# Performance work log

Measured on AMD Instinct MI355X. Metric: run time of the kernel, lower is better.

Reference implementation:

```python
import jax, jax.numpy as jnp
import numpy as np

N_ELEC = 8192   # electrons (nodes)
N_NUC = 512     # nuclei
EMB = 256       # embedding_dim
KER = 256       # kernel_dim
DF = 64         # dist_feat_dim
MID = 128       # round(sqrt(DF*KER)), log-interpolated hidden width of w-MLP
E = 131072      # edges per edge type


def _ssp(x):
    # shifted softplus, deepqmc default activation: log(0.5*exp(x) + 0.5)
    return jax.nn.softplus(x) - jnp.log(2.0)


def setup_inputs() -> dict:
    key = jax.random.key(0)
    ks = jax.random.split(key, 24)
    def nrm(k, shape, scale):
        return jax.random.normal(k, shape, dtype=jnp.float32) * scale
    inp = {}
    inp['electrons'] = nrm(ks[0], (N_ELEC, EMB), 1.0)
    inp['nuclei'] = nrm(ks[1], (N_NUC, KER), 1.0)
    for i, lbl in enumerate(['same', 'anti', 'n']):
        inp[f'dist_{lbl}'] = jax.random.uniform(ks[2 + i], (E, DF), dtype=jnp.float32)
        inp[f'w1_{lbl}'] = nrm(ks[5 + i], (DF, MID), DF ** -0.5)
        inp[f'b1_{lbl}'] = jnp.zeros((MID,), jnp.float32)
        inp[f'w2_{lbl}'] = nrm(ks[8 + i], (MID, KER), MID ** -0.5)
        inp[f'g_{lbl}'] = nrm(ks[11 + i], (KER, EMB), KER ** -0.5)
    inp['h_w'] = nrm(ks[14], (EMB, KER), EMB ** -0.5)
    inp['senders_same'] = jax.random.randint(ks[15], (E,), 0, N_ELEC)
    inp['senders_anti'] = jax.random.randint(ks[16], (E,), 0, N_ELEC)
    inp['senders_n'] = jax.random.randint(ks[17], (E,), 0, N_NUC)
    inp['receivers_same'] = jax.random.randint(ks[18], (E,), 0, N_ELEC)
    inp['receivers_anti'] = jax.random.randint(ks[19], (E,), 0, N_ELEC)
    inp['receivers_n'] = jax.random.randint(ks[20], (E,), 0, N_ELEC)
    return inp


def reference(electrons, nuclei, dist_same, dist_anti, dist_n,
              w1_same, b1_same, w2_same, w1_anti, b1_anti, w2_anti,
              w1_n, b1_n, w2_n, g_same, g_anti, g_n, h_w,
              senders_same, senders_anti, senders_n,
              receivers_same, receivers_anti, receivers_n):
    def w_mlp(d, w1, b1, w2):
        # MLP with ('log', 2) hidden layers: linear+bias -> SSP -> last linear (no bias)
        return _ssp(d @ w1 + b1) @ w2

    # per-edge filters from distance features: [E, KER]
    we_same = w_mlp(dist_same, w1_same, b1_same, w2_same)
    we_anti = w_mlp(dist_anti, w1_anti, b1_anti, w2_anti)
    we_n = w_mlp(dist_n, w1_n, b1_n, w2_n)

    # shared h (single bias-free linear) on gathered sender electrons: [E, KER]
    hx_same = electrons[senders_same] @ h_w
    hx_anti = electrons[senders_anti] @ h_w

    weh_same = we_same * hx_same
    weh_anti = we_anti * hx_anti
    weh_n = we_n * nuclei[senders_n]

    # scatter-sum messages to receiver electrons: [N_ELEC, KER]
    z_same = jax.ops.segment_sum(weh_same, receivers_same, num_segments=N_ELEC)
    z_anti = jax.ops.segment_sum(weh_anti, receivers_anti, num_segments=N_ELEC)
    z_n = jax.ops.segment_sum(weh_n, receivers_n, num_segments=N_ELEC)

    # per-label g (single bias-free linear) + residual update, order matches original
    return electrons + (z_n @ g_n + z_same @ g_same + z_anti @ g_anti)
```

## Files before the change

kernel.cpp:

```cpp
#include <hip/hip_runtime.h>
#include <stdint.h>


#define N_ELEC 8192
#define N_NUC  512
#define EMB    256
#define KER    256
#define DF     64
#define MID    128
#define NEDGE  131072
#define RPS    8256
#define CSTR   272

using u16 = unsigned short;
using u64 = unsigned long long;
typedef short short8 __attribute__((ext_vector_type(8)));
typedef float f32x4 __attribute__((ext_vector_type(4)));

__device__ __forceinline__ float bf2f(u16 h) {
  return __uint_as_float(((unsigned)h) << 16);
}
__device__ __forceinline__ u16 f2bf(float f) {
  unsigned u = __float_as_uint(f);
  return (u16)((u + 0x7FFFu + ((u >> 16) & 1u)) >> 16);
}
__device__ __forceinline__ unsigned pkbf(float a, float b) {
  return ((unsigned)f2bf(b) << 16) | (unsigned)f2bf(a);
}
__device__ __forceinline__ float ssp_fast(float x) {
  const float e = __expf(-fabsf(x));
  return fmaxf(x, 0.f) + __logf(fmaf(0.5f, e, 0.5f));
}

__device__ __forceinline__ void bar_lds() {
  __builtin_amdgcn_sched_barrier(0);
  asm volatile("s_waitcnt lgkmcnt(0)" ::: "memory");
  __builtin_amdgcn_s_barrier();
  __builtin_amdgcn_sched_barrier(0);
}

__device__ __forceinline__ void stage_t64(const char* g0, long stride,
                                          char* lds, int tid) {
  const int l = tid & 63, w = tid >> 6;
  const int r = w * 16 + (l >> 2);
  const int cb = (l & 3) * 16;
  __builtin_amdgcn_global_load_lds(
      (const __attribute__((address_space(1))) unsigned*)(g0 +
                                                          (long)r * stride +
                                                          cb),
      (__attribute__((address_space(3))) unsigned*)(lds + w * 1024), 16, 0, 0);
}
__device__ __forceinline__ void stage_f64(const float* g0, int stride_e,
                                          int kt, char* lds, int tid) {
#pragma unroll
  for (int k = 0; k < 4; ++k) {
    const int idx2 = k * 256 + tid;
    const int row = idx2 >> 4, cp = idx2 & 15;
    const float2 v = *(const float2*)(g0 + (long)row * stride_e + kt + cp * 2);
    *(unsigned*)(lds + row * 64 + cp * 4) = pkbf(v.x, v.y);
  }
}
template <bool A_F32>
__device__ __forceinline__ void gemm64(const char* A0, long as_bytes,
                                       const float* Af, int as_elems,
                                       const char* B0, long bs, int K,
                                       char* As, char* Bs, f32x4 acc[2][2],
                                       int tid) {
  const int l = tid & 63, lane15 = l & 15, quad = l >> 4, wv = tid >> 6;
  const int mw = (wv >> 1) * 32, nw = (wv & 1) * 32;
  for (int kt = 0; kt < K; kt += 32) {
    if (A_F32)
      stage_f64(Af, as_elems, kt, As, tid);
    else
      stage_t64(A0 + (long)kt * 2, as_bytes, As, tid);
    stage_t64(B0 + (long)kt * 2, bs, Bs, tid);
    __syncthreads();
    short8 af[2], bf[2];
#pragma unroll
    for (int i = 0; i < 2; ++i) {
      af[i] = *(const short8*)(As + (mw + i * 16 + lane15) * 64 + quad * 16);
      bf[i] = *(const short8*)(Bs + (nw + i * 16 + lane15) * 64 + quad * 16);
    }
#pragma unroll
    for (int mi = 0; mi < 2; ++mi)
#pragma unroll
      for (int ni = 0; ni < 2; ++ni)
        acc[mi][ni] = __builtin_amdgcn_mfma_f32_16x16x32_bf16(
            af[mi], bf[ni], acc[mi][ni], 0, 0, 0);
    __syncthreads();
  }
}

__global__ __launch_bounds__(256) void k_setup(
    const float* h_w, const float* w1s, const float* w1a, const float* w1n,
    const float* w2s, const float* w2a, const float* w2n, const float* gs,
    const float* ga, const float* gn, u16* hwT, u16* w1T, u16* w2T, u16* gT,
    float4* z, int* cnt) {
  const int b = blockIdx.x;
  if (b < 6144) {
    z[b * 256 + threadIdx.x] = (float4){0.f, 0.f, 0.f, 0.f};
    return;
  }
  if (b < 6240) {
    cnt[(b - 6144) * 256 + threadIdx.x] = 0;
    return;
  }
  int i = (b - 6240) * 256 + threadIdx.x;
  if (i < 65536) {
    int n = i >> 8, k = i & 255;
    hwT[i] = f2bf(h_w[k * 256 + n]);
    return;
  }
  int j = i - 65536;
  if (j < 24576) {
    int t = j >> 13, jj = j & 8191, n = jj >> 6, k = jj & 63;
    const float* w1 = t == 0 ? w1s : (t == 1 ? w1a : w1n);
    w1T[j] = f2bf(w1[k * 128 + n]);
    return;
  }
  j -= 24576;
  if (j < 98304) {
    int t = j >> 15, jj = j & 32767, n = jj >> 7, k = jj & 127;
    const float* w2 = t == 0 ? w2s : (t == 1 ? w2a : w2n);
    w2T[j] = f2bf(w2[k * 256 + n]);
    return;
  }
  j -= 98304;
  if (j < 196608) {
    int n = j / 768, q = j % 768, t = q >> 8, k = q & 255;
    const float* g = t == 0 ? gs : (t == 1 ? ga : gn);
    gT[j] = f2bf(g[k * 256 + n]);
  }
}

__global__ __launch_bounds__(256) void k_hist(const int* r0, const int* r1,
                                              const int* r2, int* cnt) {
  const int t = blockIdx.z;
  const int* rcv = t == 0 ? r0 : (t == 1 ? r1 : r2);
  const int e = blockIdx.x * 256 + threadIdx.x;
  atomicAdd(&cnt[t * N_ELEC + rcv[e]], 1);
}

__global__ __launch_bounds__(256) void k_scan(const int* cnt, int* rowptr,
                                              int* cursor) {
  const int t = blockIdx.x, tid = threadIdx.x;
  __shared__ int part[256];
  const int* c = cnt + t * N_ELEC;
  int s = 0;
#pragma unroll
  for (int i = 0; i < 32; ++i) s += c[tid * 32 + i];
  part[tid] = s;
  __syncthreads();
  for (int off = 1; off < 256; off <<= 1) {
    int v = (tid >= off) ? part[tid - off] : 0;
    __syncthreads();
    part[tid] += v;
    __syncthreads();
  }
  int run = (tid == 0) ? 0 : part[tid - 1];
  int* rp = rowptr + t * RPS;
  int* cu = cursor + t * N_ELEC;
  for (int i = 0; i < 32; ++i) {
    rp[tid * 32 + i] = run;
    cu[tid * 32 + i] = run;
    run += c[tid * 32 + i];
  }
  if (tid == 255) rp[N_ELEC] = run;
}

__global__ __launch_bounds__(256) void k_place(const int* r0, const int* r1,
                                               const int* r2, const int* s0,
                                               const int* s1, const int* s2,
                                               int* cursor, u64* pk) {
  const int t = blockIdx.z;
  const int* rcv = t == 0 ? r0 : (t == 1 ? r1 : r2);
  const int* snd = t == 0 ? s0 : (t == 1 ? s1 : s2);
  const int e = blockIdx.x * 256 + threadIdx.x;
  const int rr = rcv[e];
  const int pos = atomicAdd(&cursor[t * N_ELEC + rr], 1);
  pk[t * NEDGE + pos] =
      (u64)(unsigned)e | ((u64)(unsigned)snd[e] << 17) | ((u64)(unsigned)rr << 30);
}

__global__ __launch_bounds__(256) void k_he(const float* elec, const u16* hwT,
                                            u16* he) {
  __shared__ char As[4096], Bs[4096];
  f32x4 acc[2][2];
#pragma unroll
  for (int i = 0; i < 2; ++i)
#pragma unroll
    for (int j = 0; j < 2; ++j) acc[i][j] = (f32x4){0.f, 0.f, 0.f, 0.f};
  const int m0 = blockIdx.x * 64, n0 = blockIdx.y * 64;
  gemm64<true>(nullptr, 0, elec + (long)m0 * 256, 256,
               (const char*)hwT + (long)n0 * 512, 512, 256, As, Bs, acc,
               threadIdx.x);
  const int l = threadIdx.x & 63, lane15 = l & 15, quad = l >> 4,
            wv = threadIdx.x >> 6;
  const int mw = (wv >> 1) * 32, nw = (wv & 1) * 32;
#pragma unroll
  for (int mi = 0; mi < 2; ++mi)
#pragma unroll
    for (int r = 0; r < 4; ++r) {
      const int row = m0 + mw + mi * 16 + quad * 4 + r;
#pragma unroll
      for (int ni = 0; ni < 2; ++ni) {
        const int col = n0 + nw + ni * 16 + lane15;
        he[row * 256 + col] = f2bf(acc[mi][ni][r]);
      }
    }
}

__global__ __launch_bounds__(256, 5) void k_edge(
    const float* d0, const float* d1, const float* d2, const float* b0,
    const float* b1p, const float* b2, const u16* w1T, const u16* w2T,
    const u16* he, const float* nucf, const u64* pk, float* z) {
  __shared__ char mid[64 * CSTR];
  __shared__ char hc[32 * CSTR];
  __shared__ int snd_l[64], rcv_l[64];

  const int t = blockIdx.z;
  const int m0 = blockIdx.x * 64;
  const int tid = threadIdx.x;
  const float* dist = t == 0 ? d0 : (t == 1 ? d1 : d2);
  const float* bias = t == 0 ? b0 : (t == 1 ? b1p : b2);
  const u16* w1t = w1T + t * 8192;
  const u16* w2t = w2T + t * 32768;
  const bool is_nuc = (t == 2);
  const u64* pkt = pk + (size_t)t * NEDGE + m0;

  if (tid < 64) {
    const u64 rec = pkt[tid];
    snd_l[tid] = (int)((rec >> 17) & 0x1FFFu);
    rcv_l[tid] = (int)(rec >> 30);
  }

  int rows[2];
#pragma unroll
  for (int s = 0; s < 2; ++s)
    rows[s] = (int)(pkt[(s * 256 + tid) >> 3] & 0x1FFFFu);
#pragma unroll
  for (int j = 0; j < 2; ++j)
#pragma unroll
    for (int s = 0; s < 2; ++s) {
      const int idx = s * 256 + tid, row = idx >> 3, ch = idx & 7;
      const float4 v =
          *(const float4*)(dist + (long)rows[s] * 64 + j * 32 + ch * 4);
      uint2 p;
      p.x = pkbf(v.x, v.y);
      p.y = pkbf(v.z, v.w);
      *(uint2*)(mid + j * 4096 + row * 64 + ch * 8) = p;
    }
  bar_lds();

  const int l = tid & 63, lane15 = l & 15, quad = l >> 4, wv = tid >> 6;
  const int mw = (wv >> 1) * 32;
  const int nw = (wv & 1) * 64;

  f32x4 acc[2][4];
#pragma unroll
  for (int i = 0; i < 2; ++i)
#pragma unroll
    for (int j = 0; j < 4; ++j) acc[i][j] = (f32x4){0.f, 0.f, 0.f, 0.f};
#pragma unroll
  for (int j = 0; j < 2; ++j) {
    short8 af[2], bf[4];
#pragma unroll
    for (int i = 0; i < 2; ++i)
      af[i] = *(const short8*)(mid + j * 4096 + (mw + i * 16 + lane15) * 64 +
                               quad * 16);
#pragma unroll
    for (int i = 0; i < 4; ++i)
      bf[i] = *(const short8*)(w1t + (nw + i * 16 + lane15) * 64 + j * 32 +
                               quad * 8);
#pragma unroll
    for (int mi = 0; mi < 2; ++mi)
#pragma unroll
      for (int ni = 0; ni < 4; ++ni)
        acc[mi][ni] = __builtin_amdgcn_mfma_f32_16x16x32_bf16(
            af[mi], bf[ni], acc[mi][ni], 0, 0, 0);
  }
  bar_lds();

#pragma unroll
  for (int mi = 0; mi < 2; ++mi)
#pragma unroll
    for (int r = 0; r < 4; ++r) {
      const int row = mw + mi * 16 + quad * 4 + r;
#pragma unroll
      for (int ni = 0; ni < 4; ++ni) {
        const int col = nw + ni * 16 + lane15;
        const float x = acc[mi][ni][r] + bias[col];
        *(u16*)(mid + row * CSTR + col * 2) = f2bf(ssp_fast(x));
      }
    }
  bar_lds();

  for (int n0 = 0; n0 < 256; n0 += 128) {
#pragma unroll
    for (int i = 0; i < 2; ++i)
#pragma unroll
      for (int j = 0; j < 4; ++j) acc[i][j] = (f32x4){0.f, 0.f, 0.f, 0.f};
#pragma unroll
    for (int kt = 0; kt < 128; kt += 32) {
      short8 af[2], bf[4];
#pragma unroll
      for (int i = 0; i < 2; ++i)
        af[i] = *(const short8*)(mid + (mw + i * 16 + lane15) * CSTR + kt * 2 +
                                 quad * 16);
#pragma unroll
      for (int i = 0; i < 4; ++i)
        bf[i] = *(const short8*)(w2t + (n0 + nw + i * 16 + lane15) * 128 + kt +
                                 quad * 8);
#pragma unroll
      for (int mi = 0; mi < 2; ++mi)
#pragma unroll
        for (int ni = 0; ni < 4; ++ni)
          acc[mi][ni] = __builtin_amdgcn_mfma_f32_16x16x32_bf16(
              af[mi], bf[ni], acc[mi][ni], 0, 0, 0);
    }

#pragma unroll
    for (int h = 0; h < 2; ++h) {
      const int rbase = h * 32;
      if (!is_nuc) {
#pragma unroll
        for (int c = 0; c < 2; ++c) {
          const int chunk = c * 256 + tid;
          const int row = chunk >> 4, off = chunk & 15;
          const uint4 v =
              *(const uint4*)((const char*)he +
                              (size_t)snd_l[rbase + row] * 512 + n0 * 2 +
                              off * 16);
          *(uint4*)(hc + row * CSTR + off * 16) = v;
        }
      } else {
#pragma unroll
        for (int c = 0; c < 2; ++c) {
          const int chunk = c * 256 + tid;
          const int row = chunk >> 4, off = chunk & 15;
          const char* src = (const char*)nucf +
                            (size_t)snd_l[rbase + row] * 1024 + n0 * 4 +
                            off * 32;
          const float4 a = *(const float4*)src;
          const float4 b = *(const float4*)(src + 16);
          uint4 p;
          p.x = pkbf(a.x, a.y);
          p.y = pkbf(a.z, a.w);
          p.z = pkbf(b.x, b.y);
          p.w = pkbf(b.z, b.w);
          *(uint4*)(hc + row * CSTR + off * 16) = p;
        }
      }
      bar_lds();

      if ((wv >> 1) == h) {
#pragma unroll
        for (int mi = 0; mi < 2; ++mi)
#pragma unroll
          for (int r = 0; r < 4; ++r) {
            const int lrow = mi * 16 + quad * 4 + r;
#pragma unroll
            for (int ni = 0; ni < 4; ++ni) {
              const int col = nw + ni * 16 + lane15;
              u16* p = (u16*)(hc + lrow * CSTR) + col;
              *p = f2bf(acc[mi][ni][r] * bf2f(*p));
            }
          }
      }
      bar_lds();

      if (wv < 2) {
        const int cp = l;
        const int rbeg = wv * 16, rend = rbeg + 16;
        float a0 = 0.f, a1 = 0.f;
        int cur = rcv_l[rbase + rbeg];
#pragma unroll
        for (int i = 0; i < 16; ++i) {
          const int row = rbeg + i;
          const unsigned p = *(const unsigned*)(hc + row * CSTR + cp * 4);
          a0 += __uint_as_float(p << 16);
          a1 += __uint_as_float(p & 0xffff0000u);
          const int nxt = (i + 1 < 16) ? rcv_l[rbase + row + 1] : -1;
          if (nxt != cur) {
            float* zp = z + (size_t)cur * 768 + t * 256 + n0 + cp * 2;
            unsafeAtomicAdd(zp, a0);
            unsafeAtomicAdd(zp + 1, a1);
            a0 = a1 = 0.f;
            cur = nxt;
          }
        }
      }
      bar_lds();
    }
  }
}

__global__ __launch_bounds__(256) void k_final(const float* z, const u16* gT,
                                               const float* elec, float* out) {
  __shared__ char As[4096], Bs[4096];
  f32x4 acc[2][2];
#pragma unroll
  for (int i = 0; i < 2; ++i)
#pragma unroll
    for (int j = 0; j < 2; ++j) acc[i][j] = (f32x4){0.f, 0.f, 0.f, 0.f};
  const int m0 = blockIdx.x * 64, n0 = blockIdx.y * 64;
  gemm64<true>(nullptr, 0, z + (long)m0 * 768, 768,
               (const char*)gT + (long)n0 * 1536, 1536, 768, As, Bs, acc,
               threadIdx.x);
  const int l = threadIdx.x & 63, lane15 = l & 15, quad = l >> 4,
            wv = threadIdx.x >> 6;
  const int mw = (wv >> 1) * 32, nw = (wv & 1) * 32;
#pragma unroll
  for (int mi = 0; mi < 2; ++mi)
#pragma unroll
    for (int r = 0; r < 4; ++r) {
      const int row = m0 + mw + mi * 16 + quad * 4 + r;
#pragma unroll
      for (int ni = 0; ni < 2; ++ni) {
        const int col = n0 + nw + ni * 16 + lane15;
        out[row * 256 + col] = acc[mi][ni][r] + elec[row * 256 + col];
      }
    }
}

extern "C" void kernel_launch(void* const* d_in, const int* in_sizes, int n_in,
                              void* d_out, int out_size, void* d_ws,
                              size_t ws_size, hipStream_t stream) {
  int I_dist[3], I_w1[3], I_b1[3], I_w2[3], I_g[3], I_hw;
  if (in_sizes[3] == 64 * 128) {
    for (int t = 0; t < 3; ++t) {
      I_dist[t] = 2 + t * 5 + 0;
      I_w1[t] = 2 + t * 5 + 1;
      I_b1[t] = 2 + t * 5 + 2;
      I_w2[t] = 2 + t * 5 + 3;
      I_g[t] = 2 + t * 5 + 4;
    }
    I_hw = 17;
  } else {
    I_dist[0] = 2; I_dist[1] = 3; I_dist[2] = 4;
    I_w1[0] = 5;  I_b1[0] = 6;  I_w2[0] = 7;
    I_w1[1] = 8;  I_b1[1] = 9;  I_w2[1] = 10;
    I_w1[2] = 11; I_b1[2] = 12; I_w2[2] = 13;
    I_g[0] = 14; I_g[1] = 15; I_g[2] = 16;
    I_hw = 17;
  }
  const int I_snd[3] = {18, 19, 20};
  const int I_rcv[3] = {21, 22, 23};

  char* ws = (char*)d_ws;
  u16* he = (u16*)(ws + 0);
  u16* hwT = (u16*)(ws + 4194304);
  u16* w1T = (u16*)(ws + 4325376);
  u16* w2T = (u16*)(ws + 4374528);
  u16* gT = (u16*)(ws + 4571136);
  float* z = (float*)(ws + 4964352);
  int* cnt = (int*)(ws + 30130176);
  int* rowptr = (int*)(ws + 30228480);
  int* cursor = (int*)(ws + 30327552);
  u64* pk = (u64*)(ws + 30425856);

  const float* elec = (const float*)d_in[0];
  const float* nuc = (const float*)d_in[1];
  const int* s0 = (const int*)d_in[I_snd[0]];
  const int* s1 = (const int*)d_in[I_snd[1]];
  const int* s2 = (const int*)d_in[I_snd[2]];
  const int* r0 = (const int*)d_in[I_rcv[0]];
  const int* r1 = (const int*)d_in[I_rcv[1]];
  const int* r2 = (const int*)d_in[I_rcv[2]];

  k_setup<<<7744, 256, 0, stream>>>(
      (const float*)d_in[I_hw], (const float*)d_in[I_w1[0]],
      (const float*)d_in[I_w1[1]], (const float*)d_in[I_w1[2]],
      (const float*)d_in[I_w2[0]], (const float*)d_in[I_w2[1]],
      (const float*)d_in[I_w2[2]], (const float*)d_in[I_g[0]],
      (const float*)d_in[I_g[1]], (const float*)d_in[I_g[2]], hwT, w1T, w2T,
      gT, (float4*)z, cnt);

  k_hist<<<dim3(NEDGE / 256, 1, 3), 256, 0, stream>>>(r0, r1, r2, cnt);
  k_scan<<<3, 256, 0, stream>>>(cnt, rowptr, cursor);
  k_place<<<dim3(NEDGE / 256, 1, 3), 256, 0, stream>>>(r0, r1, r2, s0, s1, s2,
                                                       cursor, pk);

  k_he<<<dim3(N_ELEC / 64, 4), 256, 0, stream>>>(elec, hwT, he);

  k_edge<<<dim3(NEDGE / 64, 1, 3), 256, 0, stream>>>(
      (const float*)d_in[I_dist[0]], (const float*)d_in[I_dist[1]],
      (const float*)d_in[I_dist[2]], (const float*)d_in[I_b1[0]],
      (const float*)d_in[I_b1[1]], (const float*)d_in[I_b1[2]], w1T, w2T, he,
      nuc, pk, z);

  k_final<<<dim3(N_ELEC / 64, 4), 256, 0, stream>>>(z, gT, elec,
                                                    (float*)d_out);
}
```

Measured before the change: 412.0 us.

## Double edge tile per block and fuse sender gather into segmented scatter loop

The edge kernel now runs 512 threads on 128-edge tiles. The GEMM filter output goes into a bf16 LDS buffer once per column tile. Each wave then reads its 16 rows and directly gathers sender features from global memory (bf16 he or fp32 nuclei), multiplying with an FMA while doing the segmented atomic accumulation. This drops the staged hc buffer, the two-phase half loop, several barriers and the idle waves during the scatter, and it skips one bf16 rounding of the product. The cost is larger LDS per block, which lowers occupancy, plus narrow 4- or 8-byte uncoalesced global gathers per lane in place of 16-byte vector copies.

```diff
diff --git a/kernel.cpp b/kernel.cpp
--- a/kernel.cpp
+++ b/kernel.cpp
@@ -210,16 +210,16 @@
     }
 }
 
-__global__ __launch_bounds__(256, 5) void k_edge(
+__global__ __launch_bounds__(512, 4) void k_edge(
     const float* d0, const float* d1, const float* d2, const float* b0,
     const float* b1p, const float* b2, const u16* w1T, const u16* w2T,
     const u16* he, const float* nucf, const u64* pk, float* z) {
-  __shared__ char mid[64 * CSTR];
-  __shared__ char hc[32 * CSTR];
-  __shared__ int snd_l[64], rcv_l[64];
+  __shared__ __align__(16) char mid[128 * CSTR];
+  __shared__ __align__(16) char wec[128 * CSTR];
+  __shared__ int snd_l[128], rcv_l[128];
 
   const int t = blockIdx.z;
-  const int m0 = blockIdx.x * 64;
+  const int m0 = blockIdx.x * 128;
   const int tid = threadIdx.x;
   const float* dist = t == 0 ? d0 : (t == 1 ? d1 : d2);
   const float* bias = t == 0 ? b0 : (t == 1 ? b1p : b2);
@@ -228,7 +228,7 @@
   const bool is_nuc = (t == 2);
   const u64* pkt = pk + (size_t)t * NEDGE + m0;
 
-  if (tid < 64) {
+  if (tid < 128) {
     const u64 rec = pkt[tid];
     snd_l[tid] = (int)((rec >> 17) & 0x1FFFu);
     rcv_l[tid] = (int)(rec >> 30);
@@ -237,18 +237,18 @@
   int rows[2];
 #pragma unroll
   for (int s = 0; s < 2; ++s)
-    rows[s] = (int)(pkt[(s * 256 + tid) >> 3] & 0x1FFFFu);
+    rows[s] = (int)(pkt[(s * 512 + tid) >> 3] & 0x1FFFFu);
 #pragma unroll
   for (int j = 0; j < 2; ++j)
 #pragma unroll
     for (int s = 0; s < 2; ++s) {
-      const int idx = s * 256 + tid, row = idx >> 3, ch = idx & 7;
+      const int idx = s * 512 + tid, row = idx >> 3, ch = idx & 7;
       const float4 v =
           *(const float4*)(dist + (long)rows[s] * 64 + j * 32 + ch * 4);
       uint2 p;
       p.x = pkbf(v.x, v.y);
       p.y = pkbf(v.z, v.w);
-      *(uint2*)(mid + j * 4096 + row * 64 + ch * 8) = p;
+      *(uint2*)(mid + j * 8192 + row * 64 + ch * 8) = p;
     }
   bar_lds();
 
@@ -266,7 +266,7 @@
     short8 af[2], bf[4];
 #pragma unroll
     for (int i = 0; i < 2; ++i)
-      af[i] = *(const short8*)(mid + j * 4096 + (mw + i * 16 + lane15) * 64 +
+      af[i] = *(const short8*)(mid + j * 8192 + (mw + i * 16 + lane15) * 64 +
                                quad * 16);
 #pragma unroll
     for (int i = 0; i < 4; ++i)
@@ -320,67 +320,53 @@
     }
 
 #pragma unroll
-    for (int h = 0; h < 2; ++h) {
-      const int rbase = h * 32;
+    for (int mi = 0; mi < 2; ++mi)
+#pragma unroll
+      for (int r = 0; r < 4; ++r) {
+        const int row = mw + mi * 16 + quad * 4 + r;
+#pragma unroll
+        for (int ni = 0; ni < 4; ++ni) {
+          const int col = nw + ni * 16 + lane15;
+          *(u16*)(wec + row * CSTR + col * 2) = f2bf(acc[mi][ni][r]);
+        }
+      }
+    bar_lds();
+
+    {
+      const int cp = l;
+      const int rbeg = wv * 16;
+      float a0 = 0.f, a1 = 0.f;
+      int cur = rcv_l[rbeg];
       if (!is_nuc) {
 #pragma unroll
-        for (int c = 0; c < 2; ++c) {
-          const int chunk = c * 256 + tid;
-          const int row = chunk >> 4, off = chunk & 15;
-          const uint4 v =
-              *(const uint4*)((const char*)he +
-                              (size_t)snd_l[rbase + row] * 512 + n0 * 2 +
-                              off * 16);
-          *(uint4*)(hc + row * CSTR + off * 16) = v;
+        for (int i = 0; i < 16; ++i) {
+          const int row = rbeg + i;
+          const unsigned wp = *(const unsigned*)(wec + row * CSTR + cp * 4);
+          const unsigned hp =
+              *(const unsigned*)((const char*)he +
+                                 (size_t)snd_l[row] * 512 + n0 * 2 + cp * 4);
+          a0 = fmaf(__uint_as_float(wp << 16), __uint_as_float(hp << 16), a0);
+          a1 = fmaf(__uint_as_float(wp & 0xffff0000u),
+                    __uint_as_float(hp & 0xffff0000u), a1);
+          const int nxt = (i + 1 < 16) ? rcv_l[row + 1] : -1;
+          if (nxt != cur) {
+            float* zp = z + (size_t)cur * 768 + t * 256 + n0 + cp * 2;
+            unsafeAtomicAdd(zp, a0);
+            unsafeAtomicAdd(zp + 1, a1);
+            a0 = a1 = 0.f;
+            cur = nxt;
+          }
         }
       } else {
 #pragma unroll
-        for (int c = 0; c < 2; ++c) {
-          const int chunk = c * 256 + tid;
-          const int row = chunk >> 4, off = chunk & 15;
-          const char* src = (const char*)nucf +
-                            (size_t)snd_l[rbase + row] * 1024 + n0 * 4 +
-                            off * 32;
-          const float4 a = *(const float4*)src;
-          const float4 b = *(const float4*)(src + 16);
-          uint4 p;
-          p.x = pkbf(a.x, a.y);
-          p.y = pkbf(a.z, a.w);
-          p.z = pkbf(b.x, b.y);
-          p.w = pkbf(b.z, b.w);
-          *(uint4*)(hc + row * CSTR + off * 16) = p;
-        }
-      }
-      bar_lds();
-
-      if ((wv >> 1) == h) {
-#pragma unroll
-        for (int mi = 0; mi < 2; ++mi)
-#pragma unroll
-          for (int r = 0; r < 4; ++r) {
-            const int lrow = mi * 16 + quad * 4 + r;
-#pragma unroll
-            for (int ni = 0; ni < 4; ++ni) {
-              const int col = nw + ni * 16 + lane15;
-              u16* p = (u16*)(hc + lrow * CSTR) + col;
-              *p = f2bf(acc[mi][ni][r] * bf2f(*p));
-            }
-          }
-      }
-      bar_lds();
-
-      if (wv < 2) {
-        const int cp = l;
-        const int rbeg = wv * 16, rend = rbeg + 16;
-        float a0 = 0.f, a1 = 0.f;
-        int cur = rcv_l[rbase + rbeg];
-#pragma unroll
         for (int i = 0; i < 16; ++i) {
           const int row = rbeg + i;
-          const unsigned p = *(const unsigned*)(hc + row * CSTR + cp * 4);
-          a0 += __uint_as_float(p << 16);
-          a1 += __uint_as_float(p & 0xffff0000u);
-          const int nxt = (i + 1 < 16) ? rcv_l[rbase + row + 1] : -1;
+          const unsigned wp = *(const unsigned*)(wec + row * CSTR + cp * 4);
+          const float2 hv =
+              *(const float2*)(nucf + (size_t)snd_l[row] * 256 + n0 + cp * 2);
+          a0 = fmaf(__uint_as_float(wp << 16), hv.x, a0);
+          a1 = fmaf(__uint_as_float(wp & 0xffff0000u), hv.y, a1);
+          const int nxt = (i + 1 < 16) ? rcv_l[row + 1] : -1;
           if (nxt != cur) {
             float* zp = z + (size_t)cur * 768 + t * 256 + n0 + cp * 2;
             unsafeAtomicAdd(zp, a0);
@@ -390,8 +376,8 @@
           }
         }
       }
-      bar_lds();
-    }
+    }
+    bar_lds();
   }
 }
 
@@ -483,7 +469,7 @@
 
   k_he<<<dim3(N_ELEC / 64, 4), 256, 0, stream>>>(elec, hwT, he);
 
-  k_edge<<<dim3(NEDGE / 64, 1, 3), 256, 0, stream>>>(
+  k_edge<<<dim3(NEDGE / 128, 1, 3), 512, 0, stream>>>(
       (const float*)d_in[I_dist[0]], (const float*)d_in[I_dist[1]],
       (const float*)d_in[I_dist[2]], (const float*)d_in[I_b1[0]],
       (const float*)d_in[I_b1[1]], (const float*)d_in[I_b1[2]], w1T, w2T, he,
```

Measured after the change: 458.1 us. 11.2% more time.
